# Kernel tuning notes

Measured on AMD Instinct MI355X. Metric: run time of the kernel, lower is better.

The kernel has to match this reference:

```python
import jax, jax.numpy as jnp
import numpy as np
import itertools

DIMS = (128, 128, 128)
CHANNELS = 8
BATCH = 2_097_152


def setup_inputs() -> dict:
    key = jax.random.key(0)
    k1, k2 = jax.random.split(key)
    unList = jax.random.uniform(k1, (BATCH, len(DIMS)), dtype=jnp.float32)
    table = jax.random.uniform(k2, DIMS + (CHANNELS,), dtype=jnp.float32)  # initScale=1, initMode='R'
    return {"unList": unList, "table": table}


def reference(unList, table):
    # N-D multilinear (bilinear/trilinear) interpolated table lookup.
    dims = table.shape[:-1]
    n = len(dims)
    c = table.shape[-1]
    dims_f = jnp.asarray(dims, jnp.float32)
    # map normalized coords [0,1] onto grid [0, dim-1]
    scaled = jnp.clip(unList, 0.0, 1.0) * (dims_f - 1.0)          # [B, n]
    i0 = jnp.clip(jnp.floor(scaled), 0.0, dims_f - 2.0).astype(jnp.int32)  # lower corner
    frac = scaled - i0.astype(jnp.float32)                        # [B, n] in [0,1]
    # flatten grid for single-axis gathers
    strides = jnp.asarray([int(np.prod(dims[k + 1:])) for k in range(n)], jnp.int32)
    table_flat = table.reshape(-1, c)                             # [prod(dims), C]
    out = jnp.zeros((unList.shape[0], c), table.dtype)
    # loop over the 2^n corners (8 for 3D) -- small static loop
    for corner in itertools.product((0, 1), repeat=n):
        bits = jnp.asarray(corner, jnp.int32)                     # [n]
        flat_idx = ((i0 + bits) * strides).sum(-1)                # [B]
        w = jnp.prod(jnp.where(jnp.asarray(corner, bool), frac, 1.0 - frac), axis=-1)  # [B]
        out = out + w[:, None] * table_flat[flat_idx]             # gather + weighted sum
    return out
```

## Files before the change

kernel.cpp:

```cpp
#include <hip/hip_runtime.h>


#define DIM 128
#define CH 8
#define NBIN 4064
#define TBYTES 67108864u
#define CHUNK 8192
#define PPT 32
#define CUR_OFF 16384
#define BASE_OFF 32768
#define REC_OFF 65536

__device__ __forceinline__ int key_of(float ux, float uy) {
    float sx = fminf(fmaxf(ux, 0.0f), 1.0f) * 127.0f;
    float sy = fminf(fmaxf(uy, 0.0f), 1.0f) * 127.0f;
    int x0 = (int)fminf(floorf(sx), 126.0f);
    int y0 = (int)fminf(floorf(sy), 126.0f);
    return x0 * 32 + (y0 >> 2);
}

__global__ __launch_bounds__(256) void k_hist(const float* __restrict__ un,
                                              unsigned* __restrict__ hist, int batch) {
    __shared__ unsigned lh[NBIN];
    for (int i = threadIdx.x; i < NBIN; i += 256) lh[i] = 0;
    __syncthreads();
    int stride = gridDim.x * blockDim.x;
    for (int i = blockIdx.x * blockDim.x + threadIdx.x; i < batch; i += stride)
        atomicAdd(&lh[key_of(un[3 * i], un[3 * i + 1])], 1u);
    __syncthreads();
    for (int i = threadIdx.x; i < NBIN; i += 256)
        if (lh[i]) atomicAdd(&hist[i], lh[i]);
}

__global__ __launch_bounds__(1024) void k_scan(const unsigned* __restrict__ hist,
                                               unsigned* __restrict__ cursor,
                                               unsigned* __restrict__ base) {
    __shared__ unsigned s[1024];
    int t = threadIdx.x;
    int b0 = t * 4;
    unsigned loc[4], sum = 0;
#pragma unroll
    for (int j = 0; j < 4; ++j) {
        int k = b0 + j;
        unsigned h = (k < NBIN) ? hist[k] : 0u;
        loc[j] = sum;
        sum += h;
    }
    s[t] = sum;
    __syncthreads();
    for (int off = 1; off < 1024; off <<= 1) {
        unsigned v = (t >= off) ? s[t - off] : 0u;
        __syncthreads();
        s[t] += v;
        __syncthreads();
    }
    unsigned excl = s[t] - sum;
#pragma unroll
    for (int j = 0; j < 4; ++j) {
        int k = b0 + j;
        if (k < NBIN) { base[k] = excl + loc[j]; cursor[k] = excl + loc[j]; }
    }
    if (t == 1023) base[NBIN] = s[1023];
}

__global__ __launch_bounds__(256) void k_scatter(const float* __restrict__ un,
                                                 unsigned* __restrict__ cursor,
                                                 float4* __restrict__ rec, int batch) {
    __shared__ unsigned lh[NBIN];
    __shared__ unsigned lbase[NBIN];
    int t = threadIdx.x;
    for (int i = t; i < NBIN; i += 256) lh[i] = 0;
    __syncthreads();
    int start = blockIdx.x * CHUNK;
    unsigned kr[PPT];
#pragma unroll
    for (int j = 0; j < PPT; ++j) {
        int i = start + j * 256 + t;
        if (i < batch) {
            int k = key_of(un[3 * i], un[3 * i + 1]);
            unsigned r = atomicAdd(&lh[k], 1u);
            kr[j] = (unsigned)k | (r << 12);
        } else kr[j] = 0u;
    }
    __syncthreads();
    for (int i = t; i < NBIN; i += 256)
        lbase[i] = lh[i] ? atomicAdd(&cursor[i], lh[i]) : 0u;
    __syncthreads();
#pragma unroll
    for (int j = 0; j < PPT; ++j) {
        int i = start + j * 256 + t;
        if (i < batch) {
            unsigned k = kr[j] & 4095u, r = kr[j] >> 12;
            float ux = un[3 * i], uy = un[3 * i + 1], uz = un[3 * i + 2];
            rec[lbase[k] + r] = make_float4(ux, uy, uz, __uint_as_float((unsigned)i));
        }
    }
}

__global__ __launch_bounds__(512, 8) void k_main(const float4* __restrict__ rec,
                                                 const float* __restrict__ table,
                                                 const unsigned* __restrict__ base,
                                                 float* __restrict__ out) {
    __shared__ float4 lds4[2560];
    char* ldsb = (char*)lds4;
    const char* tb = (const char*)table;

    int g = blockIdx.x;
    int gx = g >> 5, gy2 = g & 31;
    int ybase = gy2 * 4;
    unsigned s = base[g], e = base[g + 1];

    unsigned offA = (unsigned)(gx * 128 + ybase) * 4096u;
    unsigned offB = offA + 524288u;

    int t = (int)threadIdx.x;
    int lane = t & 63, wave = t >> 6;

#pragma unroll
    for (int j = 0; j < 5; ++j) {
        int c = wave + j * 8;
        unsigned lo = (unsigned)c * 1024u;
        unsigned go = (c < 20) ? (offA + lo) : (offB + (lo - 20480u));
        go += (unsigned)lane * 16u;
        if (go > TBYTES - 16u) go = TBYTES - 16u;
        __builtin_amdgcn_global_load_lds(
            (const __attribute__((address_space(1))) void*)(tb + go),
            (__attribute__((address_space(3))) void*)(ldsb + lo), 16, 0, 0);
    }
    __syncthreads();
    if (e <= s) return;

    int p = lane >> 1, h = lane & 1;
    const float dmax = 127.0f, imax = 126.0f;
    const unsigned hoff = (unsigned)(h << 4);
    const unsigned last = e - 1u;

    unsigned myi = s + (unsigned)(wave * 32 + p);
    unsigned cnt = e - s;

#define PROC(rr, idx) { \
        if ((idx) < e) { \
            unsigned orig = __float_as_uint(rr.w); \
            float sx = fminf(fmaxf(rr.x, 0.0f), 1.0f) * dmax; \
            float sy = fminf(fmaxf(rr.y, 0.0f), 1.0f) * dmax; \
            float sz = fminf(fmaxf(rr.z, 0.0f), 1.0f) * dmax; \
            float fx0 = fminf(floorf(sx), imax); \
            float fy0 = fminf(floorf(sy), imax); \
            float fz0 = fminf(floorf(sz), imax); \
            int y0 = (int)fy0, z0 = (int)fz0; \
            float fx = sx - fx0, fy = sy - fy0, fz = sz - fz0; \
            float gxw = 1.0f - fx, gyw = 1.0f - fy, gzw = 1.0f - fz; \
            float wA0 = gxw * gyw * gzw, wA1 = gxw * gyw * fz; \
            float wB0 = gxw * fy  * gzw, wB1 = gxw * fy  * fz; \
            float wC0 = fx  * gyw * gzw, wC1 = fx  * gyw * fz; \
            float wD0 = fx  * fy  * gzw, wD1 = fx  * fy  * fz; \
            int dy = y0 - ybase; \
            unsigned a = (unsigned)(dy * 4096 + z0 * 32) + hoff; \
            float4 vA0 = *(const float4*)(ldsb + a); \
            float4 vA1 = *(const float4*)(ldsb + a + 32u); \
            float4 vB0 = *(const float4*)(ldsb + a + 4096u); \
            float4 vB1 = *(const float4*)(ldsb + a + 4128u); \
            float4 vC0 = *(const float4*)(ldsb + a + 20480u); \
            float4 vC1 = *(const float4*)(ldsb + a + 20512u); \
            float4 vD0 = *(const float4*)(ldsb + a + 24576u); \
            float4 vD1 = *(const float4*)(ldsb + a + 24608u); \
            float4 acc; \
            acc.x = wA0*vA0.x + wA1*vA1.x + wB0*vB0.x + wB1*vB1.x \
                  + wC0*vC0.x + wC1*vC1.x + wD0*vD0.x + wD1*vD1.x; \
            acc.y = wA0*vA0.y + wA1*vA1.y + wB0*vB0.y + wB1*vB1.y \
                  + wC0*vC0.y + wC1*vC1.y + wD0*vD0.y + wD1*vD1.y; \
            acc.z = wA0*vA0.z + wA1*vA1.z + wB0*vB0.z + wB1*vB1.z \
                  + wC0*vC0.z + wC1*vC1.z + wD0*vD0.z + wD1*vD1.z; \
            acc.w = wA0*vA0.w + wA1*vA1.w + wB0*vB0.w + wB1*vB1.w \
                  + wC0*vC0.w + wC1*vC1.w + wD0*vD0.w + wD1*vD1.w; \
            *reinterpret_cast<float4*>(out + (size_t)orig * CH + (h << 2)) = acc; \
        } }

    float4 r0 = rec[min(myi, last)];
    for (unsigned c0 = 0; c0 < cnt; c0 += 256u) {
        float4 n0 = rec[min(myi + c0 + 256u, last)];
        PROC(r0, myi + c0)
        r0 = n0;
    }
#undef PROC
}

__global__ __launch_bounds__(256) void k_naive(const float* __restrict__ un,
                                               const float* __restrict__ table,
                                               float* __restrict__ out, int batch) {
    int b = blockIdx.x * blockDim.x + threadIdx.x;
    if (b >= batch) return;
    float ux = un[3 * b], uy = un[3 * b + 1], uz = un[3 * b + 2];
    const float dmax = 127.0f, imax = 126.0f;
    float sx = fminf(fmaxf(ux, 0.0f), 1.0f) * dmax;
    float sy = fminf(fmaxf(uy, 0.0f), 1.0f) * dmax;
    float sz = fminf(fmaxf(uz, 0.0f), 1.0f) * dmax;
    float fx0 = fminf(floorf(sx), imax);
    float fy0 = fminf(floorf(sy), imax);
    float fz0 = fminf(floorf(sz), imax);
    int x0 = (int)fx0, y0 = (int)fy0, z0 = (int)fz0;
    float fx = sx - fx0, fy = sy - fy0, fz = sz - fz0;
    float wx[2] = {1.0f - fx, fx};
    float wy[2] = {1.0f - fy, fy};
    float wz0 = 1.0f - fz, wz1 = fz;
    float acc[CH];
#pragma unroll
    for (int c = 0; c < CH; ++c) acc[c] = 0.0f;
#pragma unroll
    for (int bx = 0; bx < 2; ++bx)
#pragma unroll
        for (int by = 0; by < 2; ++by) {
            const float* pp = table + ((size_t)((x0 + bx) * DIM + (y0 + by)) * DIM + z0) * CH;
            float wxy = wx[bx] * wy[by];
            float w0 = wxy * wz0, w1 = wxy * wz1;
            float4 a0 = *reinterpret_cast<const float4*>(pp + 0);
            float4 a1 = *reinterpret_cast<const float4*>(pp + 4);
            float4 b0 = *reinterpret_cast<const float4*>(pp + 8);
            float4 b1 = *reinterpret_cast<const float4*>(pp + 12);
            acc[0] += w0 * a0.x + w1 * b0.x;  acc[1] += w0 * a0.y + w1 * b0.y;
            acc[2] += w0 * a0.z + w1 * b0.z;  acc[3] += w0 * a0.w + w1 * b0.w;
            acc[4] += w0 * a1.x + w1 * b1.x;  acc[5] += w0 * a1.y + w1 * b1.y;
            acc[6] += w0 * a1.z + w1 * b1.z;  acc[7] += w0 * a1.w + w1 * b1.w;
        }
    float4* o = reinterpret_cast<float4*>(out + (size_t)b * CH);
    o[0] = make_float4(acc[0], acc[1], acc[2], acc[3]);
    o[1] = make_float4(acc[4], acc[5], acc[6], acc[7]);
}

extern "C" void kernel_launch(void* const* d_in, const int* in_sizes, int n_in,
                              void* d_out, int out_size, void* d_ws, size_t ws_size,
                              hipStream_t stream) {
    const float* un    = (const float*)d_in[0];
    const float* table = (const float*)d_in[1];
    float* out         = (float*)d_out;
    int batch = in_sizes[0] / 3;

    size_t need = (size_t)REC_OFF + (size_t)batch * 16;
    if (ws_size < need) {
        int grid = (batch + 255) / 256;
        k_naive<<<grid, 256, 0, stream>>>(un, table, out, batch);
        return;
    }

    unsigned* hist   = (unsigned*)d_ws;
    unsigned* cursor = (unsigned*)((char*)d_ws + CUR_OFF);
    unsigned* base   = (unsigned*)((char*)d_ws + BASE_OFF);
    float4*   rec    = (float4*)((char*)d_ws + REC_OFF);

    hipMemsetAsync(d_ws, 0, CUR_OFF, stream);
    k_hist<<<512, 256, 0, stream>>>(un, hist, batch);
    k_scan<<<1, 1024, 0, stream>>>(hist, cursor, base);
    int nscat = (batch + CHUNK - 1) / CHUNK;
    k_scatter<<<nscat, 256, 0, stream>>>(un, cursor, rec, batch);
    k_main<<<NBIN, 512, 0, stream>>>(rec, table, base, out);
}
```

Baseline: 119.5 us.

## Pack sorted records into quantized 8-byte form and widen bins to 2x4 slabs

The scatter pass now precomputes the cell offsets and quantizes the fractional coordinates to 11/11/10 bits. It packs them with the original index into an 8-byte record instead of a 16-byte float4, which halves record write and read traffic and removes coordinate math from the main kernel. Bins now cover two x-planes, so there are 2048 bins, each with a 60 KB LDS slab. This reduces duplicate table loads across blocks, and the block order is remapped for locality. In exchange, interpolation weights lose precision, batch size is capped at 2^21, and occupancy drops from 8 to 4 blocks per CU because of the larger LDS slab.

```diff
diff --git a/kernel.cpp b/kernel.cpp
--- a/kernel.cpp
+++ b/kernel.cpp
@@ -3,20 +3,21 @@
 
 #define DIM 128
 #define CH 8
-#define NBIN 4064
+#define NBIN 2048
 #define TBYTES 67108864u
 #define CHUNK 8192
 #define PPT 32
-#define CUR_OFF 16384
-#define BASE_OFF 32768
-#define REC_OFF 65536
+#define SLAB 61440
+#define CUR_OFF 8192
+#define BASE_OFF 16384
+#define REC_OFF 32768
 
 __device__ __forceinline__ int key_of(float ux, float uy) {
     float sx = fminf(fmaxf(ux, 0.0f), 1.0f) * 127.0f;
     float sy = fminf(fmaxf(uy, 0.0f), 1.0f) * 127.0f;
     int x0 = (int)fminf(floorf(sx), 126.0f);
     int y0 = (int)fminf(floorf(sy), 126.0f);
-    return x0 * 32 + (y0 >> 2);
+    return (x0 >> 1) * 32 + (y0 >> 2);
 }
 
 __global__ __launch_bounds__(256) void k_hist(const float* __restrict__ un,
@@ -37,16 +38,8 @@
                                                unsigned* __restrict__ base) {
     __shared__ unsigned s[1024];
     int t = threadIdx.x;
-    int b0 = t * 4;
-    unsigned loc[4], sum = 0;
-#pragma unroll
-    for (int j = 0; j < 4; ++j) {
-        int k = b0 + j;
-        unsigned h = (k < NBIN) ? hist[k] : 0u;
-        loc[j] = sum;
-        sum += h;
-    }
-    s[t] = sum;
+    unsigned h0 = hist[t * 2], h1 = hist[t * 2 + 1];
+    s[t] = h0 + h1;
     __syncthreads();
     for (int off = 1; off < 1024; off <<= 1) {
         unsigned v = (t >= off) ? s[t - off] : 0u;
@@ -54,18 +47,15 @@
         s[t] += v;
         __syncthreads();
     }
-    unsigned excl = s[t] - sum;
-#pragma unroll
-    for (int j = 0; j < 4; ++j) {
-        int k = b0 + j;
-        if (k < NBIN) { base[k] = excl + loc[j]; cursor[k] = excl + loc[j]; }
-    }
+    unsigned excl = s[t] - (h0 + h1);
+    base[t * 2] = excl;           cursor[t * 2] = excl;
+    base[t * 2 + 1] = excl + h0;  cursor[t * 2 + 1] = excl + h0;
     if (t == 1023) base[NBIN] = s[1023];
 }
 
 __global__ __launch_bounds__(256) void k_scatter(const float* __restrict__ un,
                                                  unsigned* __restrict__ cursor,
-                                                 float4* __restrict__ rec, int batch) {
+                                                 uint2* __restrict__ rec, int batch) {
     __shared__ unsigned lh[NBIN];
     __shared__ unsigned lbase[NBIN];
     int t = threadIdx.x;
@@ -92,70 +82,85 @@
         if (i < batch) {
             unsigned k = kr[j] & 4095u, r = kr[j] >> 12;
             float ux = un[3 * i], uy = un[3 * i + 1], uz = un[3 * i + 2];
-            rec[lbase[k] + r] = make_float4(ux, uy, uz, __uint_as_float((unsigned)i));
+            float sx = fminf(fmaxf(ux, 0.0f), 1.0f) * 127.0f;
+            float sy = fminf(fmaxf(uy, 0.0f), 1.0f) * 127.0f;
+            float sz = fminf(fmaxf(uz, 0.0f), 1.0f) * 127.0f;
+            float fx0 = fminf(floorf(sx), 126.0f);
+            float fy0 = fminf(floorf(sy), 126.0f);
+            float fz0 = fminf(floorf(sz), 126.0f);
+            int x0 = (int)fx0, y0 = (int)fy0, z0 = (int)fz0;
+            unsigned qx = (unsigned)((sx - fx0) * 2047.0f + 0.5f);
+            unsigned qy = (unsigned)((sy - fy0) * 2047.0f + 0.5f);
+            unsigned qz = (unsigned)((sz - fz0) * 1023.0f + 0.5f);
+            unsigned dx = (unsigned)(x0 & 1);
+            unsigned dy = (unsigned)(y0 & 3);
+            uint2 rr;
+            rr.x = (unsigned)i | (dx << 21) | (dy << 22) | ((unsigned)z0 << 24);
+            rr.y = qx | (qy << 11) | (qz << 22);
+            rec[lbase[k] + r] = rr;
         }
     }
 }
 
-__global__ __launch_bounds__(512, 8) void k_main(const float4* __restrict__ rec,
+__global__ __launch_bounds__(512, 4) void k_main(const uint2* __restrict__ rec,
                                                  const float* __restrict__ table,
                                                  const unsigned* __restrict__ base,
                                                  float* __restrict__ out) {
-    __shared__ float4 lds4[2560];
+    __shared__ float4 lds4[SLAB / 16];
     char* ldsb = (char*)lds4;
     const char* tb = (const char*)table;
 
-    int g = blockIdx.x;
-    int gx = g >> 5, gy2 = g & 31;
-    int ybase = gy2 * 4;
+    int pb = (int)blockIdx.x;
+    int g = (pb & 7) * 256 + (pb >> 3);
+    int X = g >> 5, Y = g & 31;
     unsigned s = base[g], e = base[g + 1];
-
-    unsigned offA = (unsigned)(gx * 128 + ybase) * 4096u;
-    unsigned offB = offA + 524288u;
 
     int t = (int)threadIdx.x;
     int lane = t & 63, wave = t >> 6;
 
 #pragma unroll
-    for (int j = 0; j < 5; ++j) {
+    for (int j = 0; j < 8; ++j) {
         int c = wave + j * 8;
-        unsigned lo = (unsigned)c * 1024u;
-        unsigned go = (c < 20) ? (offA + lo) : (offB + (lo - 20480u));
-        go += (unsigned)lane * 16u;
-        if (go > TBYTES - 16u) go = TBYTES - 16u;
-        __builtin_amdgcn_global_load_lds(
-            (const __attribute__((address_space(1))) void*)(tb + go),
-            (__attribute__((address_space(3))) void*)(ldsb + lo), 16, 0, 0);
+        if (c < 60) {
+            int pr = c >> 2, q4 = c & 3;
+            int p = (pr * 13) >> 6;
+            int r = pr - p * 5;
+            int gp = 2 * X + p;  if (gp > 127) gp = 127;
+            int gr = 4 * Y + r;  if (gr > 127) gr = 127;
+            unsigned go = (unsigned)((gp * 128 + gr) * 4096 + q4 * 1024)
+                        + (unsigned)lane * 16u;
+            __builtin_amdgcn_global_load_lds(
+                (const __attribute__((address_space(1))) void*)(tb + go),
+                (__attribute__((address_space(3))) void*)(ldsb + (unsigned)c * 1024u),
+                16, 0, 0);
+        }
     }
     __syncthreads();
     if (e <= s) return;
 
     int p = lane >> 1, h = lane & 1;
-    const float dmax = 127.0f, imax = 126.0f;
     const unsigned hoff = (unsigned)(h << 4);
     const unsigned last = e - 1u;
+    const float rs11 = 1.0f / 2047.0f, rs10 = 1.0f / 1023.0f;
 
     unsigned myi = s + (unsigned)(wave * 32 + p);
     unsigned cnt = e - s;
 
 #define PROC(rr, idx) { \
         if ((idx) < e) { \
-            unsigned orig = __float_as_uint(rr.w); \
-            float sx = fminf(fmaxf(rr.x, 0.0f), 1.0f) * dmax; \
-            float sy = fminf(fmaxf(rr.y, 0.0f), 1.0f) * dmax; \
-            float sz = fminf(fmaxf(rr.z, 0.0f), 1.0f) * dmax; \
-            float fx0 = fminf(floorf(sx), imax); \
-            float fy0 = fminf(floorf(sy), imax); \
-            float fz0 = fminf(floorf(sz), imax); \
-            int y0 = (int)fy0, z0 = (int)fz0; \
-            float fx = sx - fx0, fy = sy - fy0, fz = sz - fz0; \
+            unsigned orig = rr.x & 0x1FFFFFu; \
+            unsigned dx = (rr.x >> 21) & 1u; \
+            unsigned dy = (rr.x >> 22) & 3u; \
+            unsigned z0 = (rr.x >> 24) & 0x7Fu; \
+            float fx = (float)(rr.y & 0x7FFu) * rs11; \
+            float fy = (float)((rr.y >> 11) & 0x7FFu) * rs11; \
+            float fz = (float)(rr.y >> 22) * rs10; \
             float gxw = 1.0f - fx, gyw = 1.0f - fy, gzw = 1.0f - fz; \
             float wA0 = gxw * gyw * gzw, wA1 = gxw * gyw * fz; \
             float wB0 = gxw * fy  * gzw, wB1 = gxw * fy  * fz; \
             float wC0 = fx  * gyw * gzw, wC1 = fx  * gyw * fz; \
             float wD0 = fx  * fy  * gzw, wD1 = fx  * fy  * fz; \
-            int dy = y0 - ybase; \
-            unsigned a = (unsigned)(dy * 4096 + z0 * 32) + hoff; \
+            unsigned a = (dx * 5u + dy) * 4096u + z0 * 32u + hoff; \
             float4 vA0 = *(const float4*)(ldsb + a); \
             float4 vA1 = *(const float4*)(ldsb + a + 32u); \
             float4 vB0 = *(const float4*)(ldsb + a + 4096u); \
@@ -176,9 +181,9 @@
             *reinterpret_cast<float4*>(out + (size_t)orig * CH + (h << 2)) = acc; \
         } }
 
-    float4 r0 = rec[min(myi, last)];
+    uint2 r0 = rec[min(myi, last)];
     for (unsigned c0 = 0; c0 < cnt; c0 += 256u) {
-        float4 n0 = rec[min(myi + c0 + 256u, last)];
+        uint2 n0 = rec[min(myi + c0 + 256u, last)];
         PROC(r0, myi + c0)
         r0 = n0;
     }
@@ -235,8 +240,8 @@
     float* out         = (float*)d_out;
     int batch = in_sizes[0] / 3;
 
-    size_t need = (size_t)REC_OFF + (size_t)batch * 16;
-    if (ws_size < need) {
+    size_t need = (size_t)REC_OFF + (size_t)batch * 8;
+    if (ws_size < need || batch > (1 << 21)) {
         int grid = (batch + 255) / 256;
         k_naive<<<grid, 256, 0, stream>>>(un, table, out, batch);
         return;
@@ -245,7 +250,7 @@
     unsigned* hist   = (unsigned*)d_ws;
     unsigned* cursor = (unsigned*)((char*)d_ws + CUR_OFF);
     unsigned* base   = (unsigned*)((char*)d_ws + BASE_OFF);
-    float4*   rec    = (float4*)((char*)d_ws + REC_OFF);
+    uint2*    rec    = (uint2*)((char*)d_ws + REC_OFF);
 
     hipMemsetAsync(d_ws, 0, CUR_OFF, stream);
     k_hist<<<512, 256, 0, stream>>>(un, hist, batch);
```

Result: faster. 108.8 us (-9.0%).
